# Performance work log

Measured on AMD Instinct MI355X. Metric: run time of the kernel, lower is better.

Reference implementation:

```python
import jax, jax.numpy as jnp
import numpy as np

B, S, D, F, E, R = 16, 1024, 1024, 4096, 8, 32
LORA_ALPHA = 16
SCALING = LORA_ALPHA / R  # 0.5


def setup_inputs() -> dict:
    key = jax.random.key(0)
    ks = jax.random.split(key, 16)
    sd = 0.02
    return {
        "x": jax.random.normal(ks[0], (B, S, D), jnp.float32),
        "router_w": jax.random.normal(ks[1], (E, D), jnp.float32) * sd,
        "router_b": jnp.zeros((E,), jnp.float32),
        "fc1_w": jax.random.normal(ks[2], (F, D), jnp.float32) * sd,
        "fc1_b": jnp.zeros((F,), jnp.float32),
        "fc2_w": jax.random.normal(ks[3], (D, F), jnp.float32) * sd,
        "fc2_b": jnp.zeros((D,), jnp.float32),
        "down_A_w": jax.random.normal(ks[4], (E, R, D), jnp.float32) * sd,
        "down_A_b": jnp.zeros((E, R), jnp.float32),
        "down_B_w": jax.random.normal(ks[5], (E, F, R), jnp.float32) * sd,
        "down_B_b": jnp.zeros((E, F), jnp.float32),
        "up_A_w": jax.random.normal(ks[6], (E, R, F), jnp.float32) * sd,
        "up_A_b": jnp.zeros((E, R), jnp.float32),
        "up_B_w": jax.random.normal(ks[7], (E, D, R), jnp.float32) * sd,
        "up_B_b": jnp.zeros((E, D), jnp.float32),
    }


def _lora_moe_sparse(inp, onehot, A_w, A_b, B_w, B_b):
    # inp: [b,t,c_in]; onehot: [b,t,E] hard top-1 dispatch mask
    # h: per-expert rank activations [b,t,E,R] (small: R=32)
    h = jnp.einsum('btc,erc->bter', inp, A_w) + A_b
    g = h * onehot[..., None]  # zero out non-selected experts (sparse dispatch)
    out = jnp.einsum('bter,eor->bto', g, B_w)
    out = out + jnp.einsum('bte,eo->bto', onehot, B_b)
    return out * SCALING


def reference(x, router_w, router_b, fc1_w, fc1_b, fc2_w, fc2_b,
              down_A_w, down_A_b, down_B_w, down_B_b,
              up_A_w, up_A_b, up_B_w, up_B_b):
    # router + top-1 hard routing (straight-through expert_choice)
    logits = jnp.einsum('btd,ed->bte', x, router_w) + router_b
    routing = jax.nn.softmax(logits, axis=-1)
    idx = jnp.argmax(routing, axis=-1)                       # [b,t]
    y_hard = jax.nn.one_hot(idx, E, dtype=x.dtype)           # [b,t,E]
    expert_choice = y_hard - jax.lax.stop_gradient(routing) + routing

    # down proj: frozen fc1 + sparse LoRA combine (dropout p=0.05 -> eval/identity)
    h1 = jnp.einsum('btd,fd->btf', x, fc1_w) + fc1_b
    h1 = h1 + _lora_moe_sparse(x, y_hard, down_A_w, down_A_b, down_B_w, down_B_b)
    a = jax.nn.gelu(h1, approximate=False)

    # up proj: frozen fc2 + sparse LoRA combine
    out = jnp.einsum('btf,df->btd', a, fc2_w) + fc2_b
    out = out + _lora_moe_sparse(a, y_hard, up_A_w, up_A_b, up_B_w, up_B_b)
    return out, (routing, expert_choice)
```

## Files before the change

kernel.cpp:

```cpp
#include <hip/hip_runtime.h>
#include <hip/hip_bf16.h>
#include <math.h>


#define M_TOK 16384
#define DIM_D 1024
#define DIM_F 4096
#define NEXP 8
#define RANK 32
#define NER 256
#define K1 1280
#define K2 4352

typedef __attribute__((ext_vector_type(8))) short bf16x8;
typedef __attribute__((ext_vector_type(4))) short sh4;
typedef __attribute__((ext_vector_type(4))) float f32x4;

__device__ inline short f2bs(float x) {
  __hip_bfloat16 h = __float2bfloat16(x);
  return *reinterpret_cast<short*>(&h);
}

__device__ inline void async16(const void* g, void* l) {
  __builtin_amdgcn_global_load_lds(
      (__attribute__((address_space(1))) void*)(g),
      (__attribute__((address_space(3))) void*)(l), 16, 0, 0);
}

__device__ inline size_t pk_blk(int row, int k, int KP) {
  return (size_t)(row >> 8) * (KP >> 5) + (k >> 5);
}
__device__ inline int pk_off(int row, int k) {
  return (row & 255) * 32 + ((k & 31) ^ ((row & 8) << 1));
}

__global__ __launch_bounds__(256) void convert_packed(
    const float* __restrict__ in, short* __restrict__ out,
    int c8, int KP, int n8)
{
  const int i = blockIdx.x * 256 + threadIdx.x;
  if (i >= n8) return;
  const int row = i / c8;
  const int k = (i % c8) * 8;
  const float4* p = (const float4*)(in + (size_t)row * (c8 * 8) + k);
  float4 u = p[0], v = p[1];
  bf16x8 r;
  r[0] = f2bs(u.x); r[1] = f2bs(u.y); r[2] = f2bs(u.z); r[3] = f2bs(u.w);
  r[4] = f2bs(v.x); r[5] = f2bs(v.y); r[6] = f2bs(v.z); r[7] = f2bs(v.w);
  *(bf16x8*)(out + pk_blk(row, k, KP) * 8192 + pk_off(row, k)) = r;
}

__global__ __launch_bounds__(256) void pack_lorab(
    const float* __restrict__ in, short* __restrict__ out,
    int Nn, int KP, int ooff, int n8)
{
  const int i = blockIdx.x * 256 + threadIdx.x;
  if (i >= n8) return;
  const int e = i / (Nn * 4);
  const int rem = i % (Nn * 4);
  const int n = rem >> 2;
  const int r8 = (rem & 3) * 8;
  const int k = ooff + e * RANK + r8;
  const float4* p = (const float4*)(in + ((size_t)e * Nn + n) * RANK + r8);
  float4 u = p[0], v = p[1];
  bf16x8 r;
  r[0] = f2bs(u.x); r[1] = f2bs(u.y); r[2] = f2bs(u.z); r[3] = f2bs(u.w);
  r[4] = f2bs(v.x); r[5] = f2bs(v.y); r[6] = f2bs(v.z); r[7] = f2bs(v.w);
  *(bf16x8*)(out + pk_blk(n, k, KP) * 8192 + pk_off(n, k)) = r;
}

__global__ __launch_bounds__(256) void router_kernel(
    const float* __restrict__ X,
    const float* __restrict__ RW,
    const float* __restrict__ RB,
    float* __restrict__ routing_out,
    float* __restrict__ ec_out,
    int* __restrict__ idx_out,
    short* __restrict__ XB)
{
  const int wave = threadIdx.x >> 6;
  const int lane = threadIdx.x & 63;
  const int t = blockIdx.x * 4 + wave;

  const float4* xp = (const float4*)(X + (size_t)t * DIM_D);
  float4 xv[4];
#pragma unroll
  for (int i = 0; i < 4; ++i) xv[i] = xp[lane + 64 * i];

#pragma unroll
  for (int i = 0; i < 4; ++i) {
    sh4 o;
    o[0] = f2bs(xv[i].x); o[1] = f2bs(xv[i].y);
    o[2] = f2bs(xv[i].z); o[3] = f2bs(xv[i].w);
    const int k0 = (lane + 64 * i) * 4;
    *(sh4*)&XB[pk_blk(t, k0, K1) * 8192 + pk_off(t, k0)] = o;
  }

  float logit[NEXP];
#pragma unroll
  for (int e = 0; e < NEXP; ++e) {
    const float4* wp = (const float4*)(RW + (size_t)e * DIM_D);
    double p = 0.0;
#pragma unroll
    for (int i = 0; i < 4; ++i) {
      float4 w = wp[lane + 64 * i];
      p += (double)xv[i].x * w.x + (double)xv[i].y * w.y +
           (double)xv[i].z * w.z + (double)xv[i].w * w.w;
    }
#pragma unroll
    for (int off = 32; off > 0; off >>= 1) p += __shfl_xor(p, off);
    logit[e] = (float)p + RB[e];
  }
  float m = logit[0];
  int am = 0;
#pragma unroll
  for (int e = 1; e < NEXP; ++e)
    if (logit[e] > m) { m = logit[e]; am = e; }
  float pr[NEXP], s = 0.f;
#pragma unroll
  for (int e = 0; e < NEXP; ++e) { pr[e] = expf(logit[e] - m); s += pr[e]; }
  const float inv = 1.f / s;
  if (lane < NEXP) {
    float r = pr[lane] * inv;
    routing_out[(size_t)t * NEXP + lane] = r;
    float y = (lane == am) ? 1.f : 0.f;
    ec_out[(size_t)t * NEXP + lane] = (y - r) + r;
  }
  if (lane == 0) idx_out[t] = am;
}

template <int TM, int KA, int KB, int N, int OPK, int OOFF, int EPI>
__global__ __launch_bounds__(256, 4) void gemmT(
    const short* __restrict__ A, const short* __restrict__ Bm,
    const float* __restrict__ LB, const float* __restrict__ bias,
    const int* __restrict__ idx, void* __restrict__ outv)
{
  static_assert(TM == 64 || TM == 128, "TM");
  constexpr int NA = TM / 32;
  __shared__ __align__(16) short As[TM * 64];
  __shared__ __align__(16) short Bs[128 * 64];

  const int tid = threadIdx.x;
  const int lane = tid & 63;
  const int wv = tid >> 6;
  const int quad = lane >> 4;
  const int lrow = lane & 15;
  const int wr = wv >> 1;
  const int wc = wv & 1;
  const int swz = (quad * 8) ^ ((lrow & 8) << 1);

  const int gx = gridDim.x;
  int id = blockIdx.y * gx + blockIdx.x;
  const int nwg = gx * gridDim.y;
  id = (id & 7) * (nwg >> 3) + (id >> 3);
  const int m0 = (id / gx) * TM;
  const int n0 = (id % gx) * 128;

  f32x4 acc[NA][4];
#pragma unroll
  for (int i = 0; i < NA; ++i)
#pragma unroll
    for (int j = 0; j < 4; ++j) acc[i][j] = (f32x4){0.f, 0.f, 0.f, 0.f};

  const short* Ab = A + ((size_t)(m0 >> 8) * (KA >> 5)) * 8192 +
                    (size_t)(m0 & 255) * 32 + tid * 8;
  const short* Bb = Bm + ((size_t)(n0 >> 8) * (KB >> 5)) * 8192 +
                    (size_t)(n0 & 255) * 32 + tid * 8;

  for (int it = 0; it < KB / 64; ++it) {
#pragma unroll
    for (int kb = 0; kb < 2; ++kb) {
      if constexpr (TM == 128) {
        async16(Ab, &As[kb * 4096 + tid * 8]);
        async16(Ab + 2048, &As[kb * 4096 + tid * 8 + 2048]);
      } else {
        async16(Ab, &As[kb * 2048 + tid * 8]);
      }
      async16(Bb, &Bs[kb * 4096 + tid * 8]);
      async16(Bb + 2048, &Bs[kb * 4096 + tid * 8 + 2048]);
      Ab += 8192;
      Bb += 8192;
    }
    __syncthreads();

#pragma unroll
    for (int ks = 0; ks < 2; ++ks) {
      bf16x8 af[NA], bfv[4];
#pragma unroll
      for (int i = 0; i < NA; ++i)
        af[i] = *(const bf16x8*)&As[ks * (TM * 32) +
                                    (wr * (TM / 2) + i * 16 + lrow) * 32 + swz];
#pragma unroll
      for (int j = 0; j < 4; ++j)
        bfv[j] = *(const bf16x8*)&Bs[ks * 4096 +
                                     (wc * 64 + j * 16 + lrow) * 32 + swz];
#pragma unroll
      for (int i = 0; i < NA; ++i)
#pragma unroll
        for (int j = 0; j < 4; ++j)
          acc[i][j] = __builtin_amdgcn_mfma_f32_16x16x32_bf16(
              af[i], bfv[j], acc[i][j], 0, 0, 0);
    }
    __syncthreads();
  }

  float cb[4];
#pragma unroll
  for (int j = 0; j < 4; ++j) cb[j] = bias[n0 + wc * 64 + j * 16 + lrow];

#pragma unroll
  for (int i = 0; i < NA; ++i) {
#pragma unroll
    for (int reg = 0; reg < 4; ++reg) {
      const int t = m0 + wr * (TM / 2) + i * 16 + quad * 4 + reg;
      const int e = idx[t];
#pragma unroll
      for (int j = 0; j < 4; ++j) {
        const int gc = n0 + wc * 64 + j * 16 + lrow;
        if (EPI == 2) {
          float v = ((gc >> 5) == e) ? 0.5f * (acc[i][j][reg] + cb[j]) : 0.f;
          const int k = OOFF + gc;
          ((short*)outv)[pk_blk(t, k, OPK) * 8192 + pk_off(t, k)] = f2bs(v);
        } else {
          float v = acc[i][j][reg] + cb[j] + 0.5f * LB[(size_t)e * N + gc];
          if (EPI == 1) {
            v = 0.5f * v * (1.0f + erff(v * 0.70710678118654752f));
            const int k = OOFF + gc;
            ((short*)outv)[pk_blk(t, k, OPK) * 8192 + pk_off(t, k)] = f2bs(v);
          } else {
            ((float*)outv)[(size_t)t * OPK + gc] = v;
          }
        }
      }
    }
  }
}

extern "C" void kernel_launch(void* const* d_in, const int* in_sizes, int n_in,
                              void* d_out, int out_size, void* d_ws, size_t ws_size,
                              hipStream_t stream) {
  (void)in_sizes; (void)n_in; (void)out_size; (void)ws_size;
  const float* x        = (const float*)d_in[0];
  const float* router_w = (const float*)d_in[1];
  const float* router_b = (const float*)d_in[2];
  const float* fc1_w    = (const float*)d_in[3];
  const float* fc1_b    = (const float*)d_in[4];
  const float* fc2_w    = (const float*)d_in[5];
  const float* fc2_b    = (const float*)d_in[6];
  const float* down_A_w = (const float*)d_in[7];
  const float* down_A_b = (const float*)d_in[8];
  const float* down_B_w = (const float*)d_in[9];
  const float* down_B_b = (const float*)d_in[10];
  const float* up_A_w   = (const float*)d_in[11];
  const float* up_A_b   = (const float*)d_in[12];
  const float* up_B_w   = (const float*)d_in[13];
  const float* up_B_b   = (const float*)d_in[14];

  char* ws = (char*)d_ws;
  size_t off = 0;
  int* idxp  = (int*)ws;              off += (size_t)M_TOK * 4;
  short* xbw = (short*)(ws + off);    off += (size_t)M_TOK * K1 * 2;
  short* aw  = (short*)(ws + off);    off += (size_t)M_TOK * K2 * 2;
  short* B1w = (short*)(ws + off);    off += (size_t)DIM_F * K1 * 2;
  short* B2w = (short*)(ws + off);    off += (size_t)DIM_D * K2 * 2;
  short* dAb = (short*)(ws + off);    off += (size_t)NER * DIM_D * 2;
  short* uAb = (short*)(ws + off);    off += (size_t)NER * DIM_F * 2;

  float* out = (float*)d_out;
  float* routing = out + (size_t)M_TOK * DIM_D;
  float* ec = routing + (size_t)M_TOK * NEXP;

  convert_packed<<<2048, 256, 0, stream>>>(fc1_w, B1w, 128, K1, 524288);
  convert_packed<<<2048, 256, 0, stream>>>(fc2_w, B2w, 512, K2, 524288);
  convert_packed<<<128,  256, 0, stream>>>(down_A_w, dAb, 128, DIM_D, 32768);
  convert_packed<<<512,  256, 0, stream>>>(up_A_w,   uAb, 512, DIM_F, 131072);
  pack_lorab<<<512, 256, 0, stream>>>(down_B_w, B1w, DIM_F, K1, DIM_D, 131072);
  pack_lorab<<<128, 256, 0, stream>>>(up_B_w,   B2w, DIM_D, K2, DIM_F, 32768);

  router_kernel<<<M_TOK / 4, 256, 0, stream>>>(x, router_w, router_b, routing,
                                               ec, idxp, xbw);
  gemmT<64, K1, DIM_D, NER, K1, DIM_D, 2>
      <<<dim3(2, M_TOK / 64), 256, 0, stream>>>(
          xbw, dAb, nullptr, down_A_b, idxp, xbw);
  gemmT<128, K1, K1, DIM_F, K2, 0, 1>
      <<<dim3(DIM_F / 128, M_TOK / 128), 256, 0, stream>>>(
          xbw, B1w, down_B_b, fc1_b, idxp, aw);
  gemmT<64, K2, DIM_F, NER, K2, DIM_F, 2>
      <<<dim3(2, M_TOK / 64), 256, 0, stream>>>(
          aw, uAb, nullptr, up_A_b, idxp, aw);
  gemmT<128, K2, K2, DIM_D, DIM_D, 0, 0>
      <<<dim3(DIM_D / 128, M_TOK / 128), 256, 0, stream>>>(
          aw, B2w, up_B_b, fc2_b, idxp, out);
}
```

Baseline: 668.1 us.

## Merge weight-prep launches into one kernel and halve GEMM K-step LDS tile

Six weight conversion/packing launches are folded into a single prep_all kernel that dispatches on block index, removing launch overhead and serialization gaps between small kernels. Separately, the GEMM main loop now stages one 32-wide K slice per iteration instead of two, halving LDS usage per block. That raises potential occupancy but doubles the number of barrier pairs per K, and each barrier-bounded step now does less MFMA work to hide load latency.

```diff
diff --git a/kernel.cpp b/kernel.cpp
--- a/kernel.cpp
+++ b/kernel.cpp
@@ -34,12 +34,10 @@
   return (row & 255) * 32 + ((k & 31) ^ ((row & 8) << 1));
 }
 
-__global__ __launch_bounds__(256) void convert_packed(
-    const float* __restrict__ in, short* __restrict__ out,
-    int c8, int KP, int n8)
-{
-  const int i = blockIdx.x * 256 + threadIdx.x;
-  if (i >= n8) return;
+__device__ inline void conv_body(const float* __restrict__ in,
+                                 short* __restrict__ out,
+                                 int c8, int KP, int i)
+{
   const int row = i / c8;
   const int k = (i % c8) * 8;
   const float4* p = (const float4*)(in + (size_t)row * (c8 * 8) + k);
@@ -50,12 +48,10 @@
   *(bf16x8*)(out + pk_blk(row, k, KP) * 8192 + pk_off(row, k)) = r;
 }
 
-__global__ __launch_bounds__(256) void pack_lorab(
-    const float* __restrict__ in, short* __restrict__ out,
-    int Nn, int KP, int ooff, int n8)
-{
-  const int i = blockIdx.x * 256 + threadIdx.x;
-  if (i >= n8) return;
+__device__ inline void lorab_body(const float* __restrict__ in,
+                                  short* __restrict__ out,
+                                  int Nn, int KP, int ooff, int i)
+{
   const int e = i / (Nn * 4);
   const int rem = i % (Nn * 4);
   const int n = rem >> 2;
@@ -69,6 +65,23 @@
   *(bf16x8*)(out + pk_blk(n, k, KP) * 8192 + pk_off(n, k)) = r;
 }
 
+__global__ __launch_bounds__(256) void prep_all(
+    const float* __restrict__ fc1_w, const float* __restrict__ fc2_w,
+    const float* __restrict__ dA, const float* __restrict__ uA,
+    const float* __restrict__ dB, const float* __restrict__ uB,
+    short* __restrict__ B1w, short* __restrict__ B2w,
+    short* __restrict__ dAb, short* __restrict__ uAb)
+{
+  const int b = blockIdx.x;
+  const int t = threadIdx.x;
+  if (b < 2048)      conv_body(fc1_w, B1w, 128, K1, b * 256 + t);
+  else if (b < 4096) conv_body(fc2_w, B2w, 512, K2, (b - 2048) * 256 + t);
+  else if (b < 4224) conv_body(dA, dAb, 128, DIM_D, (b - 4096) * 256 + t);
+  else if (b < 4736) conv_body(uA, uAb, 512, DIM_F, (b - 4224) * 256 + t);
+  else if (b < 5248) lorab_body(dB, B1w, DIM_F, K1, DIM_D, (b - 4736) * 256 + t);
+  else               lorab_body(uB, B2w, DIM_D, K2, DIM_F, (b - 5248) * 256 + t);
+}
+
 __global__ __launch_bounds__(256) void router_kernel(
     const float* __restrict__ X,
     const float* __restrict__ RW,
@@ -137,8 +150,8 @@
 {
   static_assert(TM == 64 || TM == 128, "TM");
   constexpr int NA = TM / 32;
-  __shared__ __align__(16) short As[TM * 64];
-  __shared__ __align__(16) short Bs[128 * 64];
+  __shared__ __align__(16) short As[TM * 32];
+  __shared__ __align__(16) short Bs[128 * 32];
 
   const int tid = threadIdx.x;
   const int lane = tid & 63;
@@ -167,40 +180,32 @@
   const short* Bb = Bm + ((size_t)(n0 >> 8) * (KB >> 5)) * 8192 +
                     (size_t)(n0 & 255) * 32 + tid * 8;
 
-  for (int it = 0; it < KB / 64; ++it) {
-#pragma unroll
-    for (int kb = 0; kb < 2; ++kb) {
-      if constexpr (TM == 128) {
-        async16(Ab, &As[kb * 4096 + tid * 8]);
-        async16(Ab + 2048, &As[kb * 4096 + tid * 8 + 2048]);
-      } else {
-        async16(Ab, &As[kb * 2048 + tid * 8]);
-      }
-      async16(Bb, &Bs[kb * 4096 + tid * 8]);
-      async16(Bb + 2048, &Bs[kb * 4096 + tid * 8 + 2048]);
-      Ab += 8192;
-      Bb += 8192;
+  for (int it = 0; it < KB / 32; ++it) {
+    if constexpr (TM == 128) {
+      async16(Ab, &As[tid * 8]);
+      async16(Ab + 2048, &As[tid * 8 + 2048]);
+    } else {
+      async16(Ab, &As[tid * 8]);
     }
+    async16(Bb, &Bs[tid * 8]);
+    async16(Bb + 2048, &Bs[tid * 8 + 2048]);
+    Ab += 8192;
+    Bb += 8192;
     __syncthreads();
 
-#pragma unroll
-    for (int ks = 0; ks < 2; ++ks) {
-      bf16x8 af[NA], bfv[4];
-#pragma unroll
-      for (int i = 0; i < NA; ++i)
-        af[i] = *(const bf16x8*)&As[ks * (TM * 32) +
-                                    (wr * (TM / 2) + i * 16 + lrow) * 32 + swz];
+    bf16x8 af[NA], bfv[4];
+#pragma unroll
+    for (int i = 0; i < NA; ++i)
+      af[i] = *(const bf16x8*)&As[(wr * (TM / 2) + i * 16 + lrow) * 32 + swz];
+#pragma unroll
+    for (int j = 0; j < 4; ++j)
+      bfv[j] = *(const bf16x8*)&Bs[(wc * 64 + j * 16 + lrow) * 32 + swz];
+#pragma unroll
+    for (int i = 0; i < NA; ++i)
 #pragma unroll
       for (int j = 0; j < 4; ++j)
-        bfv[j] = *(const bf16x8*)&Bs[ks * 4096 +
-                                     (wc * 64 + j * 16 + lrow) * 32 + swz];
-#pragma unroll
-      for (int i = 0; i < NA; ++i)
-#pragma unroll
-        for (int j = 0; j < 4; ++j)
-          acc[i][j] = __builtin_amdgcn_mfma_f32_16x16x32_bf16(
-              af[i], bfv[j], acc[i][j], 0, 0, 0);
-    }
+        acc[i][j] = __builtin_amdgcn_mfma_f32_16x16x32_bf16(af[i], bfv[j],
+                                                            acc[i][j], 0, 0, 0);
     __syncthreads();
   }
 
@@ -270,12 +275,8 @@
   float* routing = out + (size_t)M_TOK * DIM_D;
   float* ec = routing + (size_t)M_TOK * NEXP;
 
-  convert_packed<<<2048, 256, 0, stream>>>(fc1_w, B1w, 128, K1, 524288);
-  convert_packed<<<2048, 256, 0, stream>>>(fc2_w, B2w, 512, K2, 524288);
-  convert_packed<<<128,  256, 0, stream>>>(down_A_w, dAb, 128, DIM_D, 32768);
-  convert_packed<<<512,  256, 0, stream>>>(up_A_w,   uAb, 512, DIM_F, 131072);
-  pack_lorab<<<512, 256, 0, stream>>>(down_B_w, B1w, DIM_F, K1, DIM_D, 131072);
-  pack_lorab<<<128, 256, 0, stream>>>(up_B_w,   B2w, DIM_D, K2, DIM_F, 32768);
+  prep_all<<<5376, 256, 0, stream>>>(fc1_w, fc2_w, down_A_w, up_A_w,
+                                     down_B_w, up_B_w, B1w, B2w, dAb, uAb);
 
   router_kernel<<<M_TOK / 4, 256, 0, stream>>>(x, router_w, router_b, routing,
                                                ec, idxp, xbw);
```

New measurement: 617.4 us. 1.08x faster.
